# Kernel optimization log

Measured on AMD Instinct MI355X. Metric: run time of the kernel, lower is better.

## Reference

```python
import jax, jax.numpy as jnp
import numpy as np

STRIDE = 1

def setup_inputs() -> dict:
    key = jax.random.key(0)
    k1, k2, k3 = jax.random.split(key, 3)
    x = jax.random.normal(k1, (32, 64, 112, 112), dtype=jnp.float32)
    weight = jax.random.normal(k2, (128, 64, 3, 3), dtype=jnp.float32)
    bias = jax.random.normal(k3, (128,), dtype=jnp.float32)
    return {"x": x, "weight": weight, "bias": bias}

def reference(x, weight, bias):
    # Naive per-patch multiply-sum conv == standard cross-correlation conv2d,
    # stride=1, no padding (VALID).  x: (N,Cin,H,W), weight: (Cout,Cin,kH,kW)
    out = jax.lax.conv_general_dilated(
        x, weight,
        window_strides=(STRIDE, STRIDE),
        padding="VALID",
        dimension_numbers=("NCHW", "OIHW", "NCHW"),
    )
    return out + bias[None, :, None, None]
```

## Files before the change

kernel.cpp:

```cpp
#include <hip/hip_runtime.h>
#include <hip/hip_bf16.h>


#define CIN   64
#define COUT  128
#define INH   112
#define INW   112
#define OUTH  110
#define OUTW  110
#define NB    32
#define KTOT  576
#define NPIX  (NB*OUTH*OUTW)

typedef __attribute__((ext_vector_type(8))) short short8;
typedef __attribute__((ext_vector_type(4))) float f32x4;

static __device__ __forceinline__ unsigned short f2bf(float f) {
    union { float f; unsigned int u; } v; v.f = f;
    return (unsigned short)((v.u + 0x7FFF + ((v.u >> 16) & 1)) >> 16);
}

__global__ __launch_bounds__(256) void prepack_w(const float* __restrict__ w,
                                                 unsigned short* __restrict__ ap) {
    int flat = blockIdx.x * 256 + threadIdx.x;
    int m = flat / KTOT;
    int k = flat - m * KTOT;
    int khw = k >> 6, ci = k & 63;
    int kh = khw / 3, kw = khw - kh * 3;
    float v = w[((m * CIN + ci) * 3 + kh) * 3 + kw];
    ap[((k >> 3) * COUT + m) * 8 + (k & 7)] = f2bf(v);
}

__global__ __launch_bounds__(256, 3) void conv_gemm(const float* __restrict__ x,
                                                    const unsigned short* __restrict__ ap,
                                                    const float* __restrict__ bias,
                                                    float* __restrict__ out) {
    __shared__ unsigned short ldsB[25600];

    const int flat0 = blockIdx.y * OUTH + blockIdx.x;
    const int flat  = (flat0 & 7) * 440 + (flat0 >> 3);
    const int n  = flat / OUTH;
    const int oh = flat - n * OUTH;
    const int t  = threadIdx.x;

    const int lane = t & 63;
    const int wave = t >> 6;
    const int m_base  = (wave >> 1) * 64;
    const int px_base = (wave & 1) * 64;
    const int l16  = lane & 15;
    const int quad = lane >> 4;

    const short8* A = (const short8*)ap;

    auto loadA = [&](short8* a, int kc) {
#pragma unroll
        for (int i = 0; i < 4; ++i)
            a[i] = A[(kc * 4 + quad) * COUT + (m_base + i * 16 + l16)];
    };
    auto loadB = [&](short8* b, int kc) {
        const int khw = kc >> 1;
        const int kh = khw / 3, kw = khw - kh * 3;
        const int ci0 = (kc & 1) * 32 + quad * 8;
#pragma unroll
        for (int j = 0; j < 4; ++j) {
            int ow = px_base + j * 16 + l16;
            b[j] = *(const short8*)&ldsB[(kh * INW + ow + kw) * 72 + ci0];
        }
    };

    short8 a0[4], a1[4], b0[4], b1[4];
    loadA(a0, 0);

    {
        const float* xb = x + ((size_t)n * CIN) * (INH * INW) + (size_t)oh * INW;
        for (int c = t; c < 5376; c += 256) {
            int w2 = c % 56;
            int rest = c / 56;
            int cip = rest & 31, r = rest >> 5;
            const float* p = xb + (size_t)(2 * cip) * (INH * INW) + r * INW + 2 * w2;
            float2 va = *(const float2*)p;
            float2 vb = *(const float2*)(p + INH * INW);
            unsigned int d0 = (unsigned int)f2bf(va.x) | ((unsigned int)f2bf(vb.x) << 16);
            unsigned int d1 = (unsigned int)f2bf(va.y) | ((unsigned int)f2bf(vb.y) << 16);
            int cell = r * INW + 2 * w2;
            *(unsigned int*)&ldsB[cell * 72 + 2 * cip] = d0;
            *(unsigned int*)&ldsB[(cell + 1) * 72 + 2 * cip] = d1;
        }
    }
    loadA(a1, 1);
    __syncthreads();

    f32x4 acc[4][4] = {};
    loadB(b0, 0);
    loadB(b1, 1);

#pragma unroll
    for (int kc = 0; kc < 18; kc += 2) {
#pragma unroll
        for (int i = 0; i < 4; ++i)
#pragma unroll
            for (int j = 0; j < 4; ++j)
                acc[i][j] = __builtin_amdgcn_mfma_f32_16x16x32_bf16(a0[i], b0[j], acc[i][j], 0, 0, 0);
        if (kc + 2 < 18) { loadA(a0, kc + 2); loadB(b0, kc + 2); }
#pragma unroll
        for (int i = 0; i < 4; ++i)
#pragma unroll
            for (int j = 0; j < 4; ++j)
                acc[i][j] = __builtin_amdgcn_mfma_f32_16x16x32_bf16(a1[i], b1[j], acc[i][j], 0, 0, 0);
        if (kc + 3 < 18) { loadA(a1, kc + 3); loadB(b1, kc + 3); }
    }

#pragma unroll
    for (int i = 0; i < 4; ++i) {
        const int co = m_base + i * 16 + quad * 4;
#pragma unroll
        for (int j = 0; j < 4; ++j) {
            const int ow = px_base + j * 16 + l16;
            if (ow < OUTW) {
                const size_t ob = (((size_t)n * COUT + co) * OUTH + oh) * OUTW + ow;
#pragma unroll
                for (int r = 0; r < 4; ++r)
                    out[ob + (size_t)r * (OUTH * OUTW)] = acc[i][j][r] + bias[co + r];
            }
        }
    }
}

#define TCO 16
__global__ __launch_bounds__(256) void conv_direct(const float* __restrict__ x,
                                                   const float* __restrict__ w,
                                                   const float* __restrict__ bias,
                                                   float* __restrict__ out) {
    int p = blockIdx.x * 256 + threadIdx.x;
    const int co0 = blockIdx.y * TCO;
    const bool valid = p < NPIX;
    if (!valid) p = 0;
    const int n = p / (OUTH * OUTW);
    const int rem = p - n * (OUTH * OUTW);
    const int oh = rem / OUTW;
    const int ow = rem - oh * OUTW;
    float acc[TCO];
#pragma unroll
    for (int t = 0; t < TCO; ++t) acc[t] = bias[co0 + t];
    const float* xb = x + ((size_t)n * CIN) * (INH * INW) + (size_t)oh * INW + ow;
    const float* wb = w + (size_t)co0 * CIN * 9;
    for (int ci = 0; ci < CIN; ++ci) {
        const float* xp = xb + (size_t)ci * (INH * INW);
        const float* wp = wb + ci * 9;
#pragma unroll
        for (int kh = 0; kh < 3; ++kh) {
            const float x0 = xp[kh * INW + 0];
            const float x1 = xp[kh * INW + 1];
            const float x2 = xp[kh * INW + 2];
#pragma unroll
            for (int t = 0; t < TCO; ++t) {
                const float* wt = wp + t * (CIN * 9) + kh * 3;
                acc[t] = fmaf(x0, wt[0], acc[t]);
                acc[t] = fmaf(x1, wt[1], acc[t]);
                acc[t] = fmaf(x2, wt[2], acc[t]);
            }
        }
    }
    if (valid) {
        const size_t ob = ((size_t)n * COUT + co0) * (OUTH * OUTW) + (size_t)oh * OUTW + ow;
#pragma unroll
        for (int t = 0; t < TCO; ++t)
            out[ob + (size_t)t * (OUTH * OUTW)] = acc[t];
    }
}

extern "C" void kernel_launch(void* const* d_in, const int* in_sizes, int n_in,
                              void* d_out, int out_size, void* d_ws, size_t ws_size,
                              hipStream_t stream) {
    const float* x    = (const float*)d_in[0];
    const float* w    = (const float*)d_in[1];
    const float* bias = (const float*)d_in[2];
    float* out        = (float*)d_out;

    const size_t ap_bytes = (size_t)COUT * KTOT * 2;

    if (ws_size >= ap_bytes) {
        unsigned short* apck = (unsigned short*)d_ws;
        prepack_w<<<288, 256, 0, stream>>>(w, apck);
        conv_gemm<<<dim3(OUTH, NB), 256, 0, stream>>>(x, apck, bias, out);
    } else {
        dim3 grid((NPIX + 255) / 256, COUT / TCO);
        conv_direct<<<grid, dim3(256), 0, stream>>>(x, w, bias, out);
    }
}
```

Baseline: 370.3 us.

## Compute two output rows per block with larger per-wave pixel tile

Each block now computes two output rows instead of one, staging four input rows (shared halo) in LDS. Each wave covers 128 pixels with a 4x8 accumulator array, reusing its A fragments across twice as many MFMAs. The input staging loop is rewritten with a per-lane channel/cell mapping, and MFMA groups are wrapped in s_setprio. Occupancy drops from 3 to 2 blocks per CU because of the larger LDS tile and more accumulator registers.

```diff
diff --git a/kernel.cpp b/kernel.cpp
--- a/kernel.cpp
+++ b/kernel.cpp
@@ -1,11 +1,11 @@
 #include <hip/hip_runtime.h>
-#include <hip/hip_bf16.h>
 
 
 #define CIN   64
 #define COUT  128
 #define INH   112
 #define INW   112
+#define HW    (INH*INW)
 #define OUTH  110
 #define OUTW  110
 #define NB    32
@@ -31,22 +31,23 @@
     ap[((k >> 3) * COUT + m) * 8 + (k & 7)] = f2bf(v);
 }
 
-__global__ __launch_bounds__(256, 3) void conv_gemm(const float* __restrict__ x,
+__global__ __launch_bounds__(256, 2) void conv_gemm(const float* __restrict__ x,
                                                     const unsigned short* __restrict__ ap,
                                                     const float* __restrict__ bias,
                                                     float* __restrict__ out) {
-    __shared__ unsigned short ldsB[25600];
-
-    const int flat0 = blockIdx.y * OUTH + blockIdx.x;
-    const int flat  = (flat0 & 7) * 440 + (flat0 >> 3);
-    const int n  = flat / OUTH;
-    const int oh = flat - n * OUTH;
-    const int t  = threadIdx.x;
+    __shared__ unsigned short ldsB[32256];
+
+    const int flat0 = blockIdx.y * 55 + blockIdx.x;
+    const int flat  = (flat0 & 7) * 220 + (flat0 >> 3);
+    const int n   = flat / 55;
+    const int ohp = flat - n * 55;
+    const int oh0 = ohp * 2;
+    const int t   = threadIdx.x;
 
     const int lane = t & 63;
-    const int wave = t >> 6;
-    const int m_base  = (wave >> 1) * 64;
-    const int px_base = (wave & 1) * 64;
+    const int wv   = t >> 6;
+    const int m_base  = (wv >> 1) * 64;
+    const int px_base = (wv & 1) * 128;
     const int l16  = lane & 15;
     const int quad = lane >> 4;
 
@@ -57,67 +58,92 @@
         for (int i = 0; i < 4; ++i)
             a[i] = A[(kc * 4 + quad) * COUT + (m_base + i * 16 + l16)];
     };
-    auto loadB = [&](short8* b, int kc) {
+    auto loadBh = [&](short8* b, int kc, int h) {
         const int khw = kc >> 1;
         const int kh = khw / 3, kw = khw - kh * 3;
         const int ci0 = (kc & 1) * 32 + quad * 8;
 #pragma unroll
-        for (int j = 0; j < 4; ++j) {
-            int ow = px_base + j * 16 + l16;
-            b[j] = *(const short8*)&ldsB[(kh * INW + ow + kw) * 72 + ci0];
+        for (int jj = 0; jj < 4; ++jj) {
+            int px = px_base + (h * 4 + jj) * 16 + l16;
+            int orow = px >> 7;
+            int ow = px & 127;
+            ow = (ow < OUTW) ? ow : (OUTW - 1);
+            b[jj] = *(const short8*)&ldsB[((orow + kh) * INW + ow + kw) * 72 + ci0];
         }
     };
 
-    short8 a0[4], a1[4], b0[4], b1[4];
+    short8 a0[4], a1[4], bA[4], bB[4];
     loadA(a0, 0);
 
     {
-        const float* xb = x + ((size_t)n * CIN) * (INH * INW) + (size_t)oh * INW;
-        for (int c = t; c < 5376; c += 256) {
-            int w2 = c % 56;
-            int rest = c / 56;
-            int cip = rest & 31, r = rest >> 5;
-            const float* p = xb + (size_t)(2 * cip) * (INH * INW) + r * INW + 2 * w2;
-            float2 va = *(const float2*)p;
-            float2 vb = *(const float2*)(p + INH * INW);
-            unsigned int d0 = (unsigned int)f2bf(va.x) | ((unsigned int)f2bf(vb.x) << 16);
-            unsigned int d1 = (unsigned int)f2bf(va.y) | ((unsigned int)f2bf(vb.y) << 16);
-            int cell = r * INW + 2 * w2;
-            *(unsigned int*)&ldsB[cell * 72 + 2 * cip] = d0;
-            *(unsigned int*)&ldsB[(cell + 1) * 72 + 2 * cip] = d1;
+        const int cq  = lane & 7;
+        const int cip = wv * 8 + ((lane >> 3) & 3) + 4 * (lane >> 5);
+        const float* p0 = x + ((size_t)n * CIN + 2 * cip) * HW + (size_t)oh0 * INW;
+        unsigned int* ldsW = (unsigned int*)ldsB;
+#pragma unroll 8
+        for (int i = 0; i < 56; ++i) {
+            int cell = i * 8 + cq;
+            int r = cell / 112, w = cell - r * 112;
+            float va = p0[r * INW + w];
+            float vb = p0[HW + r * INW + w];
+            ldsW[cell * 36 + cip] = (unsigned int)f2bf(va) | ((unsigned int)f2bf(vb) << 16);
         }
     }
     loadA(a1, 1);
     __syncthreads();
 
-    f32x4 acc[4][4] = {};
-    loadB(b0, 0);
-    loadB(b1, 1);
+    f32x4 acc[4][8] = {};
+    loadBh(bA, 0, 0);
 
 #pragma unroll
     for (int kc = 0; kc < 18; kc += 2) {
-#pragma unroll
-        for (int i = 0; i < 4; ++i)
-#pragma unroll
-            for (int j = 0; j < 4; ++j)
-                acc[i][j] = __builtin_amdgcn_mfma_f32_16x16x32_bf16(a0[i], b0[j], acc[i][j], 0, 0, 0);
-        if (kc + 2 < 18) { loadA(a0, kc + 2); loadB(b0, kc + 2); }
-#pragma unroll
-        for (int i = 0; i < 4; ++i)
-#pragma unroll
-            for (int j = 0; j < 4; ++j)
-                acc[i][j] = __builtin_amdgcn_mfma_f32_16x16x32_bf16(a1[i], b1[j], acc[i][j], 0, 0, 0);
-        if (kc + 3 < 18) { loadA(a1, kc + 3); loadB(b1, kc + 3); }
+        loadBh(bB, kc, 1);
+        __builtin_amdgcn_s_setprio(1);
+#pragma unroll
+        for (int i = 0; i < 4; ++i)
+#pragma unroll
+            for (int jj = 0; jj < 4; ++jj)
+                acc[i][jj] = __builtin_amdgcn_mfma_f32_16x16x32_bf16(a0[i], bA[jj], acc[i][jj], 0, 0, 0);
+        __builtin_amdgcn_s_setprio(0);
+        loadBh(bA, kc + 1, 0);
+        __builtin_amdgcn_s_setprio(1);
+#pragma unroll
+        for (int i = 0; i < 4; ++i)
+#pragma unroll
+            for (int jj = 0; jj < 4; ++jj)
+                acc[i][4 + jj] = __builtin_amdgcn_mfma_f32_16x16x32_bf16(a0[i], bB[jj], acc[i][4 + jj], 0, 0, 0);
+        __builtin_amdgcn_s_setprio(0);
+        if (kc + 2 < 18) loadA(a0, kc + 2);
+
+        loadBh(bB, kc + 1, 1);
+        __builtin_amdgcn_s_setprio(1);
+#pragma unroll
+        for (int i = 0; i < 4; ++i)
+#pragma unroll
+            for (int jj = 0; jj < 4; ++jj)
+                acc[i][jj] = __builtin_amdgcn_mfma_f32_16x16x32_bf16(a1[i], bA[jj], acc[i][jj], 0, 0, 0);
+        __builtin_amdgcn_s_setprio(0);
+        if (kc + 2 < 18) loadBh(bA, kc + 2, 0);
+        __builtin_amdgcn_s_setprio(1);
+#pragma unroll
+        for (int i = 0; i < 4; ++i)
+#pragma unroll
+            for (int jj = 0; jj < 4; ++jj)
+                acc[i][4 + jj] = __builtin_amdgcn_mfma_f32_16x16x32_bf16(a1[i], bB[jj], acc[i][4 + jj], 0, 0, 0);
+        __builtin_amdgcn_s_setprio(0);
+        if (kc + 3 < 18) loadA(a1, kc + 3);
     }
 
 #pragma unroll
     for (int i = 0; i < 4; ++i) {
         const int co = m_base + i * 16 + quad * 4;
 #pragma unroll
-        for (int j = 0; j < 4; ++j) {
-            const int ow = px_base + j * 16 + l16;
+        for (int j = 0; j < 8; ++j) {
+            const int px = px_base + j * 16 + l16;
+            const int orow = px >> 7;
+            const int ow = px & 127;
             if (ow < OUTW) {
-                const size_t ob = (((size_t)n * COUT + co) * OUTH + oh) * OUTW + ow;
+                const size_t ob = (((size_t)n * COUT + co) * OUTH + (oh0 + orow)) * OUTW + ow;
 #pragma unroll
                 for (int r = 0; r < 4; ++r)
                     out[ob + (size_t)r * (OUTH * OUTW)] = acc[i][j][r] + bias[co + r];
@@ -142,10 +168,10 @@
     float acc[TCO];
 #pragma unroll
     for (int t = 0; t < TCO; ++t) acc[t] = bias[co0 + t];
-    const float* xb = x + ((size_t)n * CIN) * (INH * INW) + (size_t)oh * INW + ow;
+    const float* xb = x + ((size_t)n * CIN) * HW + (size_t)oh * INW + ow;
     const float* wb = w + (size_t)co0 * CIN * 9;
     for (int ci = 0; ci < CIN; ++ci) {
-        const float* xp = xb + (size_t)ci * (INH * INW);
+        const float* xp = xb + (size_t)ci * HW;
         const float* wp = wb + ci * 9;
 #pragma unroll
         for (int kh = 0; kh < 3; ++kh) {
@@ -182,7 +208,7 @@
     if (ws_size >= ap_bytes) {
         unsigned short* apck = (unsigned short*)d_ws;
         prepack_w<<<288, 256, 0, stream>>>(w, apck);
-        conv_gemm<<<dim3(OUTH, NB), 256, 0, stream>>>(x, apck, bias, out);
+        conv_gemm<<<dim3(55, NB), 256, 0, stream>>>(x, apck, bias, out);
     } else {
         dim3 grid((NPIX + 255) / 256, COUT / TCO);
         conv_direct<<<grid, dim3(256), 0, stream>>>(x, w, bias, out);
```

After: 324.9 us. 12.3% less time.

## Process bands of output rows per block with a rolling LDS input-row buffer

Applied to the files above, without the earlier changes.

Each block now computes a band of up to 7 output rows instead of a single row, holding a 4-slot ring of bf16-converted input rows in LDS. This means each input row is loaded and converted once per band rather than three times (once per kernel row). The next row's global loads are issued ahead of the MFMA loop and written to LDS after the epilogue, so the fetch overlaps compute. MFMA sections also get raised wave priority. The cost is a grid of only 512 blocks at 2 blocks per CU, which may underfill the GPU and leave the last band with fewer rows than the others.

```diff
diff --git a/kernel.cpp b/kernel.cpp
--- a/kernel.cpp
+++ b/kernel.cpp
@@ -1,16 +1,19 @@
 #include <hip/hip_runtime.h>
-#include <hip/hip_bf16.h>
 
 
 #define CIN   64
 #define COUT  128
 #define INH   112
 #define INW   112
+#define HW    (INH*INW)
 #define OUTH  110
 #define OUTW  110
 #define NB    32
 #define KTOT  576
 #define NPIX  (NB*OUTH*OUTW)
+#define NBANDS 16
+#define RPB   7
+#define SLOT  8064
 
 typedef __attribute__((ext_vector_type(8))) short short8;
 typedef __attribute__((ext_vector_type(4))) float f32x4;
@@ -31,98 +34,136 @@
     ap[((k >> 3) * COUT + m) * 8 + (k & 7)] = f2bf(v);
 }
 
-__global__ __launch_bounds__(256, 3) void conv_gemm(const float* __restrict__ x,
+__global__ __launch_bounds__(256, 2) void conv_gemm(const float* __restrict__ x,
                                                     const unsigned short* __restrict__ ap,
                                                     const float* __restrict__ bias,
                                                     float* __restrict__ out) {
-    __shared__ unsigned short ldsB[25600];
-
-    const int flat0 = blockIdx.y * OUTH + blockIdx.x;
-    const int flat  = (flat0 & 7) * 440 + (flat0 >> 3);
-    const int n  = flat / OUTH;
-    const int oh = flat - n * OUTH;
-    const int t  = threadIdx.x;
-
+    __shared__ unsigned short ldsB[4 * SLOT];
+
+    const int flat0 = blockIdx.y * NBANDS + blockIdx.x;
+    const int flat  = (flat0 & 7) * 64 + (flat0 >> 3);
+    const int n    = flat >> 4;
+    const int band = flat & 15;
+    const int oh0  = band * RPB;
+    const int nr   = (band == NBANDS - 1) ? (OUTH - RPB * (NBANDS - 1)) : RPB;
+
+    const int t    = threadIdx.x;
     const int lane = t & 63;
-    const int wave = t >> 6;
-    const int m_base  = (wave >> 1) * 64;
-    const int px_base = (wave & 1) * 64;
+    const int wv   = t >> 6;
+    const int m_base  = (wv >> 1) * 64;
+    const int px_base = (wv & 1) * 64;
     const int l16  = lane & 15;
     const int quad = lane >> 4;
 
     const short8* A = (const short8*)ap;
+
+    const int cq  = lane & 7;
+    const int cip = wv * 8 + ((lane >> 3) & 3) + 4 * (lane >> 5);
+    const float* xrow0 = x + ((size_t)n * CIN + 2 * cip) * HW + (size_t)oh0 * INW;
+    unsigned int* ldsW = (unsigned int*)ldsB;
+
+    auto stageIssue = [&](float2* st, int r) {
+        const float* p = xrow0 + (size_t)r * INW;
+#pragma unroll
+        for (int i = 0; i < 7; ++i) {
+            int w0 = 16 * i + 2 * cq;
+            st[2 * i]     = *(const float2*)(p + w0);
+            st[2 * i + 1] = *(const float2*)(p + HW + w0);
+        }
+    };
+    auto stageWrite = [&](const float2* st, int slot) {
+        unsigned int* dst = ldsW + slot * (SLOT / 2) + cip;
+#pragma unroll
+        for (int i = 0; i < 7; ++i) {
+            int w0 = 16 * i + 2 * cq;
+            float2 va = st[2 * i], vb = st[2 * i + 1];
+            dst[(w0)     * 36] = (unsigned int)f2bf(va.x) | ((unsigned int)f2bf(vb.x) << 16);
+            dst[(w0 + 1) * 36] = (unsigned int)f2bf(va.y) | ((unsigned int)f2bf(vb.y) << 16);
+        }
+    };
 
     auto loadA = [&](short8* a, int kc) {
 #pragma unroll
         for (int i = 0; i < 4; ++i)
             a[i] = A[(kc * 4 + quad) * COUT + (m_base + i * 16 + l16)];
     };
-    auto loadB = [&](short8* b, int kc) {
-        const int khw = kc >> 1;
-        const int kh = khw / 3, kw = khw - kh * 3;
-        const int ci0 = (kc & 1) * 32 + quad * 8;
-#pragma unroll
-        for (int j = 0; j < 4; ++j) {
-            int ow = px_base + j * 16 + l16;
-            b[j] = *(const short8*)&ldsB[(kh * INW + ow + kw) * 72 + ci0];
-        }
-    };
 
     short8 a0[4], a1[4], b0[4], b1[4];
+    float2 st[14];
+
     loadA(a0, 0);
-
-    {
-        const float* xb = x + ((size_t)n * CIN) * (INH * INW) + (size_t)oh * INW;
-        for (int c = t; c < 5376; c += 256) {
-            int w2 = c % 56;
-            int rest = c / 56;
-            int cip = rest & 31, r = rest >> 5;
-            const float* p = xb + (size_t)(2 * cip) * (INH * INW) + r * INW + 2 * w2;
-            float2 va = *(const float2*)p;
-            float2 vb = *(const float2*)(p + INH * INW);
-            unsigned int d0 = (unsigned int)f2bf(va.x) | ((unsigned int)f2bf(vb.x) << 16);
-            unsigned int d1 = (unsigned int)f2bf(va.y) | ((unsigned int)f2bf(vb.y) << 16);
-            int cell = r * INW + 2 * w2;
-            *(unsigned int*)&ldsB[cell * 72 + 2 * cip] = d0;
-            *(unsigned int*)&ldsB[(cell + 1) * 72 + 2 * cip] = d1;
-        }
+    for (int r = 0; r < 3; ++r) {
+        stageIssue(st, r);
+        stageWrite(st, r);
     }
     loadA(a1, 1);
     __syncthreads();
 
-    f32x4 acc[4][4] = {};
-    loadB(b0, 0);
-    loadB(b1, 1);
-
-#pragma unroll
-    for (int kc = 0; kc < 18; kc += 2) {
-#pragma unroll
-        for (int i = 0; i < 4; ++i)
-#pragma unroll
-            for (int j = 0; j < 4; ++j)
-                acc[i][j] = __builtin_amdgcn_mfma_f32_16x16x32_bf16(a0[i], b0[j], acc[i][j], 0, 0, 0);
-        if (kc + 2 < 18) { loadA(a0, kc + 2); loadB(b0, kc + 2); }
-#pragma unroll
-        for (int i = 0; i < 4; ++i)
-#pragma unroll
-            for (int j = 0; j < 4; ++j)
-                acc[i][j] = __builtin_amdgcn_mfma_f32_16x16x32_bf16(a1[i], b1[j], acc[i][j], 0, 0, 0);
-        if (kc + 3 < 18) { loadA(a1, kc + 3); loadB(b1, kc + 3); }
-    }
-
-#pragma unroll
-    for (int i = 0; i < 4; ++i) {
-        const int co = m_base + i * 16 + quad * 4;
-#pragma unroll
-        for (int j = 0; j < 4; ++j) {
-            const int ow = px_base + j * 16 + l16;
-            if (ow < OUTW) {
-                const size_t ob = (((size_t)n * COUT + co) * OUTH + oh) * OUTW + ow;
-#pragma unroll
-                for (int r = 0; r < 4; ++r)
-                    out[ob + (size_t)r * (OUTH * OUTW)] = acc[i][j][r] + bias[co + r];
+    for (int r = 0; r < nr; ++r) {
+        const bool doStage = (r + 3 < nr + 2);
+        if (doStage) stageIssue(st, r + 3);
+
+        const int sb0 = ((r    ) & 3) * SLOT;
+        const int sb1 = ((r + 1) & 3) * SLOT;
+        const int sb2 = ((r + 2) & 3) * SLOT;
+
+        auto loadB = [&](short8* b, int kc) {
+            const int khw = kc >> 1;
+            const int kh = khw / 3, kw = khw - kh * 3;
+            const int sb = (kh == 0) ? sb0 : (kh == 1) ? sb1 : sb2;
+            const int ci0 = (kc & 1) * 32 + quad * 8;
+#pragma unroll
+            for (int j = 0; j < 4; ++j) {
+                int ow = px_base + j * 16 + l16;
+                ow = (ow < OUTW) ? ow : (OUTW - 1);
+                b[j] = *(const short8*)&ldsB[sb + (ow + kw) * 72 + ci0];
             }
-        }
+        };
+
+        f32x4 acc[4][4] = {};
+        loadB(b0, 0);
+        loadB(b1, 1);
+
+#pragma unroll
+        for (int kc = 0; kc < 18; kc += 2) {
+            __builtin_amdgcn_s_setprio(1);
+#pragma unroll
+            for (int i = 0; i < 4; ++i)
+#pragma unroll
+                for (int j = 0; j < 4; ++j)
+                    acc[i][j] = __builtin_amdgcn_mfma_f32_16x16x32_bf16(a0[i], b0[j], acc[i][j], 0, 0, 0);
+            __builtin_amdgcn_s_setprio(0);
+            if (kc + 2 < 18) { loadA(a0, kc + 2); loadB(b0, kc + 2); }
+            else             { loadA(a0, 0); }
+            __builtin_amdgcn_s_setprio(1);
+#pragma unroll
+            for (int i = 0; i < 4; ++i)
+#pragma unroll
+                for (int j = 0; j < 4; ++j)
+                    acc[i][j] = __builtin_amdgcn_mfma_f32_16x16x32_bf16(a1[i], b1[j], acc[i][j], 0, 0, 0);
+            __builtin_amdgcn_s_setprio(0);
+            if (kc + 3 < 18) { loadA(a1, kc + 3); loadB(b1, kc + 3); }
+            else             { loadA(a1, 1); }
+        }
+
+        const int ohr = oh0 + r;
+#pragma unroll
+        for (int i = 0; i < 4; ++i) {
+            const int co = m_base + i * 16 + quad * 4;
+#pragma unroll
+            for (int j = 0; j < 4; ++j) {
+                const int ow = px_base + j * 16 + l16;
+                if (ow < OUTW) {
+                    const size_t ob = (((size_t)n * COUT + co) * OUTH + ohr) * OUTW + ow;
+#pragma unroll
+                    for (int rr = 0; rr < 4; ++rr)
+                        out[ob + (size_t)rr * (OUTH * OUTW)] = acc[i][j][rr] + bias[co + rr];
+                }
+            }
+        }
+
+        if (doStage) stageWrite(st, (r + 3) & 3);
+        __syncthreads();
     }
 }
 
@@ -142,10 +183,10 @@
     float acc[TCO];
 #pragma unroll
     for (int t = 0; t < TCO; ++t) acc[t] = bias[co0 + t];
-    const float* xb = x + ((size_t)n * CIN) * (INH * INW) + (size_t)oh * INW + ow;
+    const float* xb = x + ((size_t)n * CIN) * HW + (size_t)oh * INW + ow;
     const float* wb = w + (size_t)co0 * CIN * 9;
     for (int ci = 0; ci < CIN; ++ci) {
-        const float* xp = xb + (size_t)ci * (INH * INW);
+        const float* xp = xb + (size_t)ci * HW;
         const float* wp = wb + ci * 9;
 #pragma unroll
         for (int kh = 0; kh < 3; ++kh) {
@@ -182,7 +223,7 @@
     if (ws_size >= ap_bytes) {
         unsigned short* apck = (unsigned short*)d_ws;
         prepack_w<<<288, 256, 0, stream>>>(w, apck);
-        conv_gemm<<<dim3(OUTH, NB), 256, 0, stream>>>(x, apck, bias, out);
+        conv_gemm<<<dim3(NBANDS, NB), 256, 0, stream>>>(x, apck, bias, out);
     } else {
         dim3 grid((NPIX + 255) / 256, COUT / TCO);
         conv_direct<<<grid, dim3(256), 0, stream>>>(x, w, bias, out);
```

Result: slower. 528.1 us (+42.6%).
